# Kernel tuning notes

Hardware: AMD Instinct MI355X
Metric: run time of the kernel (lower is better)

## Reference

```python
import jax, jax.numpy as jnp
import numpy as np

HEADS = 8


def setup_inputs() -> dict:
    key = jax.random.key(0)
    k1, k2, k3 = jax.random.split(key, 3)
    b, n, d = 4, 2048, 256
    x = jax.random.normal(k1, (b, n, d), dtype=jnp.float32)
    # torch Linear weight is [out, in]; we store transposed [in, out] for x @ W
    w_qkv = jax.random.normal(k2, (d, 3 * d), dtype=jnp.float32) * (d ** -0.5)
    b_qkv = jnp.zeros((3 * d,), dtype=jnp.float32)
    w_out = jax.random.normal(k3, (d, d), dtype=jnp.float32) * (d ** -0.5)
    b_out = jnp.zeros((d,), dtype=jnp.float32)
    return {"x": x, "w_qkv": w_qkv, "b_qkv": b_qkv, "w_out": w_out, "b_out": b_out}


def reference(x, w_qkv, b_qkv, w_out, b_out):
    b, n, d = x.shape
    h = HEADS
    dh = d // h
    scale = d ** -0.5  # NOTE: original scales by full dim**-0.5, not head_dim
    qkv = x @ w_qkv + b_qkv                      # [b, n, 3d]
    q, k, v = jnp.split(qkv, 3, axis=-1)         # each [b, n, d]
    to_heads = lambda t: t.reshape(b, n, h, dh).transpose(0, 2, 1, 3)  # [b,h,n,dh]
    q, k, v = to_heads(q), to_heads(k), to_heads(v)
    dots = jnp.einsum('bhid,bhjd->bhij', q, k) * scale   # [b,h,n,n]
    attn = jax.nn.softmax(dots, axis=-1)
    out = jnp.einsum('bhij,bhjd->bhid', attn, v)         # [b,h,n,dh]
    out = out.transpose(0, 2, 1, 3).reshape(b, n, d)     # [b,n,d]
    return out @ w_out + b_out  # dropout is identity in eval mode
```

## Files before the change

kernel.cpp:

```cpp
#include <hip/hip_runtime.h>
#include <hip/hip_bf16.h>
#include <math.h>

#define BATCH  4
#define SEQ    2048
#define DMODEL 256
#define NH     8
#define DH     32
#define MTOT   (BATCH*SEQ)
#define QSCALE 0.09016844005556021f

typedef short  bf16x8 __attribute__((ext_vector_type(8)));
typedef float  f32x4  __attribute__((ext_vector_type(4)));

static __device__ __forceinline__ ushort f2bf(float f) {
    __hip_bfloat16 h = __float2bfloat16(f);
    return __builtin_bit_cast(ushort, h);
}

static __device__ __forceinline__ uint rne2(float a, float b) {
    uint ua = __builtin_bit_cast(uint, a);
    uint ub = __builtin_bit_cast(uint, b);
    ua += 0x7FFFu + ((ua >> 16) & 1u);
    ub += 0x7FFFu + ((ub >> 16) & 1u);
    return __builtin_amdgcn_perm(ub, ua, 0x07060302);
}

__global__ __launch_bounds__(256) void wcvt_all(
    const float* __restrict__ wq, const float* __restrict__ wo,
    const float* __restrict__ x,
    ushort* __restrict__ wqT, ushort* __restrict__ woT,
    ushort* __restrict__ xbf)
{
    const int t  = threadIdx.x;
    const int bx = blockIdx.x;
    if (bx >= 32) {
        const size_t base = ((size_t)(bx - 32) * 8 + blockIdx.y) * 4096 + t * 16;
        float4 f0 = *(const float4*)(x + base);
        float4 f1 = *(const float4*)(x + base + 4);
        float4 f2 = *(const float4*)(x + base + 8);
        float4 f3 = *(const float4*)(x + base + 12);
        uint4 w0, w1;
        w0.x = rne2(f0.x, f0.y); w0.y = rne2(f0.z, f0.w);
        w0.z = rne2(f1.x, f1.y); w0.w = rne2(f1.z, f1.w);
        w1.x = rne2(f2.x, f2.y); w1.y = rne2(f2.z, f2.w);
        w1.z = rne2(f3.x, f3.y); w1.w = rne2(f3.z, f3.w);
        *(uint4*)&xbf[base]     = w0;
        *(uint4*)&xbf[base + 8] = w1;
        return;
    }
    __shared__ float T[32][33];
    const float* w; ushort* wT; int N, n0;
    if (bx < 24) { w = wq; wT = wqT; N = 768; n0 = bx * 32; }
    else         { w = wo; wT = woT; N = 256; n0 = (bx - 24) * 32; }
    const int k0 = blockIdx.y * 32;
    {
        int tr = t >> 3, tc = (t & 7) * 4;
        *(float4*)&T[tr][tc] = *(const float4*)(w + (size_t)(k0 + tr) * N + n0 + tc);
    }
    __syncthreads();
    int nl = t >> 3, kq = (t & 7) * 4;
    ushort4 pk;
    pk.x = f2bf(T[kq + 0][nl]); pk.y = f2bf(T[kq + 1][nl]);
    pk.z = f2bf(T[kq + 2][nl]); pk.w = f2bf(T[kq + 3][nl]);
    *(ushort4*)&wT[(size_t)(n0 + nl) * 256 + k0 + kq] = pk;
}

#define LSQ 72

__global__ __launch_bounds__(256, 3) void qkv_gemm(
    const ushort* __restrict__ xb_, const ushort* __restrict__ wT,
    const float* __restrict__ bias,
    ushort* __restrict__ qo, ushort* __restrict__ ko, ushort* __restrict__ vo)
{
    __shared__ ushort As[64 * LSQ];
    __shared__ ushort Bs[128 * LSQ];
    const int tid  = threadIdx.x;
    const int wid  = tid >> 6;
    const int lane = tid & 63;
    const int lq   = lane & 15;
    const int quad = lane >> 4;
    const int wm   = wid & 1;
    const int wn   = wid >> 1;
    const int m0   = blockIdx.y * 64;
    const int n0   = blockIdx.x * 128;
    const bool isV = (blockIdx.x >= 4);

    const int ar0 = tid >> 3,         ac0 = (tid & 7) * 8;
    const int ar1 = (tid + 256) >> 3, ac1 = ac0;
    const int br0 = tid >> 3,         bc0 = (tid & 7) * 8;
    const int br1 = (tid + 256) >> 3, bc1 = bc0;
    const int br2 = (tid + 512) >> 3, bc2 = bc0;
    const int br3 = (tid + 768) >> 3, bc3 = bc0;

    const ushort* xb = xb_ + (size_t)m0 * 256;
    const ushort* wb = wT  + (size_t)n0 * 256;

    f32x4 acc[8];
#pragma unroll
    for (int i = 0; i < 8; ++i) acc[i] = {0.f, 0.f, 0.f, 0.f};

    uint4 ra0 = *(const uint4*)(xb + (size_t)ar0 * 256 + ac0);
    uint4 ra1 = *(const uint4*)(xb + (size_t)ar1 * 256 + ac1);
    uint4 rb0 = *(const uint4*)(wb + (size_t)br0 * 256 + bc0);
    uint4 rb1 = *(const uint4*)(wb + (size_t)br1 * 256 + bc1);
    uint4 rb2 = *(const uint4*)(wb + (size_t)br2 * 256 + bc2);
    uint4 rb3 = *(const uint4*)(wb + (size_t)br3 * 256 + bc3);

    for (int k0 = 0; k0 < 256; k0 += 64) {
        __syncthreads();
        *(uint4*)&As[ar0 * LSQ + ac0] = ra0;
        *(uint4*)&As[ar1 * LSQ + ac1] = ra1;
        *(uint4*)&Bs[br0 * LSQ + bc0] = rb0;
        *(uint4*)&Bs[br1 * LSQ + bc1] = rb1;
        *(uint4*)&Bs[br2 * LSQ + bc2] = rb2;
        *(uint4*)&Bs[br3 * LSQ + bc3] = rb3;
        __syncthreads();

        const int kn = (k0 + 64) & 255;
        ra0 = *(const uint4*)(xb + (size_t)ar0 * 256 + kn + ac0);
        ra1 = *(const uint4*)(xb + (size_t)ar1 * 256 + kn + ac1);
        rb0 = *(const uint4*)(wb + (size_t)br0 * 256 + kn + bc0);
        rb1 = *(const uint4*)(wb + (size_t)br1 * 256 + kn + bc1);
        rb2 = *(const uint4*)(wb + (size_t)br2 * 256 + kn + bc2);
        rb3 = *(const uint4*)(wb + (size_t)br3 * 256 + kn + bc3);

#pragma unroll
        for (int kh = 0; kh < 2; ++kh) {
            bf16x8 af[2], bfg[4];
#pragma unroll
            for (int mi = 0; mi < 2; ++mi)
                af[mi]  = *(const bf16x8*)&As[(wm * 32 + mi * 16 + lq) * LSQ + kh * 32 + quad * 8];
#pragma unroll
            for (int ni = 0; ni < 4; ++ni)
                bfg[ni] = *(const bf16x8*)&Bs[(wn * 64 + ni * 16 + lq) * LSQ + kh * 32 + quad * 8];
            if (isV) {
#pragma unroll
                for (int mi = 0; mi < 2; ++mi)
#pragma unroll
                    for (int ni = 0; ni < 4; ++ni)
                        acc[mi * 4 + ni] = __builtin_amdgcn_mfma_f32_16x16x32_bf16(
                            af[mi], bfg[ni], acc[mi * 4 + ni], 0, 0, 0);
            } else {
#pragma unroll
                for (int ni = 0; ni < 4; ++ni)
#pragma unroll
                    for (int mi = 0; mi < 2; ++mi)
                        acc[ni * 2 + mi] = __builtin_amdgcn_mfma_f32_16x16x32_bf16(
                            bfg[ni], af[mi], acc[ni * 2 + mi], 0, 0, 0);
            }
        }
    }

    if (!isV) {
#pragma unroll
        for (int ni = 0; ni < 4; ++ni) {
            int nb = n0 + wn * 64 + ni * 16 + quad * 4;
            float4 bs = *(const float4*)(bias + nb);
            int h   = (nb >> 5) & 7;
            int dh0 = nb & 31;
            bool  isQ = (nb < 256);
            float sc  = isQ ? QSCALE : 1.0f;
            ushort* dst = isQ ? qo : ko;
#pragma unroll
            for (int mi = 0; mi < 2; ++mi) {
                int m   = m0 + wm * 32 + mi * 16 + lq;
                int b   = m >> 11, seq = m & 2047;
                f32x4 c = acc[ni * 2 + mi];
                ushort4 pk;
                pk.x = f2bf((c[0] + bs.x) * sc); pk.y = f2bf((c[1] + bs.y) * sc);
                pk.z = f2bf((c[2] + bs.z) * sc); pk.w = f2bf((c[3] + bs.w) * sc);
                *(ushort4*)&dst[(((size_t)b * NH + h) * SEQ + seq) * DH + dh0] = pk;
            }
        }
    } else {
#pragma unroll
        for (int ni = 0; ni < 4; ++ni) {
            int n  = n0 + wn * 64 + ni * 16 + lq;
            int h  = (n >> 5) & 7;
            int dh = n & 31;
            float bsc = bias[n];
#pragma unroll
            for (int mi = 0; mi < 2; ++mi) {
                int mb  = m0 + wm * 32 + mi * 16 + quad * 4;
                int b   = mb >> 11, seq = mb & 2047;
                f32x4 c = acc[mi * 4 + ni];
                ushort4 pk;
                pk.x = f2bf(c[0] + bsc); pk.y = f2bf(c[1] + bsc);
                pk.z = f2bf(c[2] + bsc); pk.w = f2bf(c[3] + bsc);
                *(ushort4*)&vo[(((size_t)b * NH + h) * DH + dh) * SEQ + seq] = pk;
            }
        }
    }
}

#define KS_STRIDE 40
#define VT_STRIDE 136
#define P_STRIDE  136

__global__ __launch_bounds__(256, 4) void attn_mfma(
    const ushort* __restrict__ qb, const ushort* __restrict__ kb,
    const ushort* __restrict__ vtb, ushort* __restrict__ a_bf)
{
    __shared__ ushort Ks[128 * KS_STRIDE];
    __shared__ ushort VsT[32 * VT_STRIDE];
    __shared__ ushort Pl[4 * 32 * P_STRIDE];

    const int tid  = threadIdx.x;
    const int wid  = tid >> 6;
    const int lane = tid & 63;
    const int lq   = lane & 15;
    const int quad = lane >> 4;
    const int h    = blockIdx.y;
    const int b    = blockIdx.z;
    const int bh   = b * NH + h;
    const int q0   = blockIdx.x * 128 + wid * 32;

    const ushort* qbase = qb + ((size_t)bh * SEQ + q0) * DH;
    const bf16x8 qf0 = *(const bf16x8*)(qbase + (size_t)lq * DH + quad * 8);
    const bf16x8 qf1 = *(const bf16x8*)(qbase + (size_t)(16 + lq) * DH + quad * 8);

    const ushort* kbase  = kb  + (size_t)bh * SEQ * DH;
    const ushort* vtbase = vtb + (size_t)bh * DH * SEQ;
    ushort* Pw = Pl + wid * 32 * P_STRIDE;

    const int f0 = tid, f1 = tid + 256;
    const int kgo0 = (f0 >> 2) * DH + (f0 & 3) * 8;
    const int kgo1 = (f1 >> 2) * DH + (f1 & 3) * 8;
    const int klo0 = (f0 >> 2) * KS_STRIDE + (f0 & 3) * 8;
    const int klo1 = (f1 >> 2) * KS_STRIDE + (f1 & 3) * 8;
    const int vgo0 = (f0 >> 4) * SEQ + (f0 & 15) * 8;
    const int vgo1 = (f1 >> 4) * SEQ + (f1 & 15) * 8;
    const int vlo0 = (f0 >> 4) * VT_STRIDE + (f0 & 15) * 8;
    const int vlo1 = (f1 >> 4) * VT_STRIDE + (f1 & 15) * 8;

    uint4 kr0 = *(const uint4*)(kbase  + kgo0);
    uint4 kr1 = *(const uint4*)(kbase  + kgo1);
    uint4 vr0 = *(const uint4*)(vtbase + vgo0);
    uint4 vr1 = *(const uint4*)(vtbase + vgo1);

    f32x4 o0 = {0.f, 0.f, 0.f, 0.f};
    f32x4 o1 = {0.f, 0.f, 0.f, 0.f};
    f32x4 o2 = {0.f, 0.f, 0.f, 0.f};
    f32x4 o3 = {0.f, 0.f, 0.f, 0.f};
    float l0 = 0.f, l1 = 0.f;

    for (int kt = 0; kt < SEQ; kt += 128) {
        __syncthreads();
        *(uint4*)&Ks[klo0]  = kr0;
        *(uint4*)&Ks[klo1]  = kr1;
        *(uint4*)&VsT[vlo0] = vr0;
        *(uint4*)&VsT[vlo1] = vr1;
        __syncthreads();

        {
            const int ktn = (kt + 128) & (SEQ - 1);
            const ushort* kn = kbase  + (size_t)ktn * DH;
            const ushort* vn = vtbase + ktn;
            kr0 = *(const uint4*)(kn + kgo0);
            kr1 = *(const uint4*)(kn + kgo1);
            vr0 = *(const uint4*)(vn + vgo0);
            vr1 = *(const uint4*)(vn + vgo1);
        }

        {
            f32x4 st[8];
#pragma unroll
            for (int t = 0; t < 8; ++t) {
                bf16x8 kf = *(const bf16x8*)&Ks[(t * 16 + lq) * KS_STRIDE + quad * 8];
                f32x4 z = {0.f, 0.f, 0.f, 0.f};
                st[t] = __builtin_amdgcn_mfma_f32_16x16x32_bf16(kf, qf0, z, 0, 0, 0);
            }
#pragma unroll
            for (int t = 0; t < 8; ++t) {
                float p0 = __builtin_amdgcn_exp2f(st[t][0]);
                float p1 = __builtin_amdgcn_exp2f(st[t][1]);
                float p2 = __builtin_amdgcn_exp2f(st[t][2]);
                float p3 = __builtin_amdgcn_exp2f(st[t][3]);
                l0 += (p0 + p1) + (p2 + p3);
                uint2 w;
                w.x = rne2(p0, p1);
                w.y = rne2(p2, p3);
                *(uint2*)&Pw[lq * P_STRIDE + t * 16 + quad * 4] = w;
            }
        }
        {
            f32x4 st[8];
#pragma unroll
            for (int t = 0; t < 8; ++t) {
                bf16x8 kf = *(const bf16x8*)&Ks[(t * 16 + lq) * KS_STRIDE + quad * 8];
                f32x4 z = {0.f, 0.f, 0.f, 0.f};
                st[t] = __builtin_amdgcn_mfma_f32_16x16x32_bf16(kf, qf1, z, 0, 0, 0);
            }
#pragma unroll
            for (int t = 0; t < 8; ++t) {
                float p0 = __builtin_amdgcn_exp2f(st[t][0]);
                float p1 = __builtin_amdgcn_exp2f(st[t][1]);
                float p2 = __builtin_amdgcn_exp2f(st[t][2]);
                float p3 = __builtin_amdgcn_exp2f(st[t][3]);
                l1 += (p0 + p1) + (p2 + p3);
                uint2 w;
                w.x = rne2(p0, p1);
                w.y = rne2(p2, p3);
                *(uint2*)&Pw[(16 + lq) * P_STRIDE + t * 16 + quad * 4] = w;
            }
        }

#pragma unroll
        for (int s = 0; s < 4; ++s) {
            bf16x8 v0 = *(const bf16x8*)&VsT[lq        * VT_STRIDE + s * 32 + quad * 8];
            bf16x8 v1 = *(const bf16x8*)&VsT[(16 + lq) * VT_STRIDE + s * 32 + quad * 8];
            bf16x8 p0 = *(const bf16x8*)&Pw[lq        * P_STRIDE + s * 32 + quad * 8];
            bf16x8 p1 = *(const bf16x8*)&Pw[(16 + lq) * P_STRIDE + s * 32 + quad * 8];
            o0 = __builtin_amdgcn_mfma_f32_16x16x32_bf16(v0, p0, o0, 0, 0, 0);
            o1 = __builtin_amdgcn_mfma_f32_16x16x32_bf16(v1, p0, o1, 0, 0, 0);
            o2 = __builtin_amdgcn_mfma_f32_16x16x32_bf16(v0, p1, o2, 0, 0, 0);
            o3 = __builtin_amdgcn_mfma_f32_16x16x32_bf16(v1, p1, o3, 0, 0, 0);
        }
    }

    l0 += __shfl_xor(l0, 16); l0 += __shfl_xor(l0, 32);
    l1 += __shfl_xor(l1, 16); l1 += __shfl_xor(l1, 32);
    float inv0 = 1.0f / l0;
    float inv1 = 1.0f / l1;
    ushort* dst0 = a_bf + ((size_t)b * SEQ + q0 + lq) * DMODEL + h * DH;
    ushort* dst1 = dst0 + 16 * DMODEL;
    uint2 w0, w1;
    w0.x = rne2(o0[0] * inv0, o0[1] * inv0);
    w0.y = rne2(o0[2] * inv0, o0[3] * inv0);
    w1.x = rne2(o1[0] * inv0, o1[1] * inv0);
    w1.y = rne2(o1[2] * inv0, o1[3] * inv0);
    *(uint2*)&dst0[quad * 4]      = w0;
    *(uint2*)&dst0[16 + quad * 4] = w1;
    w0.x = rne2(o2[0] * inv1, o2[1] * inv1);
    w0.y = rne2(o2[2] * inv1, o2[3] * inv1);
    w1.x = rne2(o3[0] * inv1, o3[1] * inv1);
    w1.y = rne2(o3[2] * inv1, o3[3] * inv1);
    *(uint2*)&dst1[quad * 4]      = w0;
    *(uint2*)&dst1[16 + quad * 4] = w1;
}

__global__ __launch_bounds__(256) void out_gemm(
    const ushort* __restrict__ a, const ushort* __restrict__ wT,
    const float* __restrict__ bias, float* __restrict__ out)
{
    __shared__ ushort As[64 * LSQ];
    __shared__ ushort Bs[64 * LSQ];
    const int tid  = threadIdx.x;
    const int wid  = tid >> 6;
    const int lane = tid & 63;
    const int lq   = lane & 15;
    const int quad = lane >> 4;
    const int wm   = wid & 1;
    const int wn   = wid >> 1;
    const int m0   = blockIdx.y * 64;
    const int n0   = blockIdx.x * 64;

    const int f0 = tid, f1 = tid + 256;
    const int r0 = f0 >> 3, c0 = (f0 & 7) * 8;
    const int r1 = f1 >> 3, c1 = (f1 & 7) * 8;

    const ushort* ab = a  + (size_t)m0 * 256;
    const ushort* wb = wT + (size_t)n0 * 256;

    f32x4 acc[4];
#pragma unroll
    for (int i = 0; i < 4; ++i) acc[i] = {0.f, 0.f, 0.f, 0.f};

    uint4 ra0 = *(const uint4*)(ab + (size_t)r0 * 256 + c0);
    uint4 ra1 = *(const uint4*)(ab + (size_t)r1 * 256 + c1);
    uint4 rb0 = *(const uint4*)(wb + (size_t)r0 * 256 + c0);
    uint4 rb1 = *(const uint4*)(wb + (size_t)r1 * 256 + c1);

    for (int k0 = 0; k0 < 256; k0 += 64) {
        __syncthreads();
        *(uint4*)&As[r0 * LSQ + c0] = ra0;
        *(uint4*)&As[r1 * LSQ + c1] = ra1;
        *(uint4*)&Bs[r0 * LSQ + c0] = rb0;
        *(uint4*)&Bs[r1 * LSQ + c1] = rb1;
        __syncthreads();

        const int kn = (k0 + 64) & 255;
        ra0 = *(const uint4*)(ab + (size_t)r0 * 256 + kn + c0);
        ra1 = *(const uint4*)(ab + (size_t)r1 * 256 + kn + c1);
        rb0 = *(const uint4*)(wb + (size_t)r0 * 256 + kn + c0);
        rb1 = *(const uint4*)(wb + (size_t)r1 * 256 + kn + c1);

#pragma unroll
        for (int kh = 0; kh < 2; ++kh) {
            bf16x8 af[2], bfg[2];
#pragma unroll
            for (int mi = 0; mi < 2; ++mi)
                af[mi]  = *(const bf16x8*)&As[(wm * 32 + mi * 16 + lq) * LSQ + kh * 32 + quad * 8];
#pragma unroll
            for (int ni = 0; ni < 2; ++ni)
                bfg[ni] = *(const bf16x8*)&Bs[(wn * 32 + ni * 16 + lq) * LSQ + kh * 32 + quad * 8];
#pragma unroll
            for (int ni = 0; ni < 2; ++ni)
#pragma unroll
                for (int mi = 0; mi < 2; ++mi)
                    acc[ni * 2 + mi] = __builtin_amdgcn_mfma_f32_16x16x32_bf16(
                        bfg[ni], af[mi], acc[ni * 2 + mi], 0, 0, 0);
        }
    }

#pragma unroll
    for (int ni = 0; ni < 2; ++ni) {
        int nb = n0 + wn * 32 + ni * 16 + quad * 4;
        float4 bs = *(const float4*)(bias + nb);
#pragma unroll
        for (int mi = 0; mi < 2; ++mi) {
            int m = m0 + wm * 32 + mi * 16 + lq;
            f32x4 c = acc[ni * 2 + mi];
            float4 o;
            o.x = c[0] + bs.x; o.y = c[1] + bs.y;
            o.z = c[2] + bs.z; o.w = c[3] + bs.w;
            *(float4*)&out[(size_t)m * DMODEL + nb] = o;
        }
    }
}

extern "C" void kernel_launch(void* const* d_in, const int* in_sizes, int n_in,
                              void* d_out, int out_size, void* d_ws, size_t ws_size,
                              hipStream_t stream) {
    const float* x     = (const float*)d_in[0];
    const float* w_qkv = (const float*)d_in[1];
    const float* b_qkv = (const float*)d_in[2];
    const float* w_out = (const float*)d_in[3];
    const float* b_out = (const float*)d_in[4];
    float* out = (float*)d_out;

    const size_t TSZ = (size_t)MTOT * DMODEL;
    ushort* q_ws = (ushort*)d_ws;
    ushort* k_ws = q_ws + TSZ;
    ushort* v_ws = k_ws + TSZ;
    ushort* a_bf = v_ws + TSZ;
    ushort* xbf  = a_bf + TSZ;
    ushort* wqT  = xbf + TSZ;
    ushort* woT  = wqT + 768 * 256;

    wcvt_all<<<dim3(96, 8), 256, 0, stream>>>(w_qkv, w_out, x, wqT, woT, xbf);
    qkv_gemm<<<dim3(6, 128), 256, 0, stream>>>(xbf, wqT, b_qkv, q_ws, k_ws, v_ws);
    attn_mfma<<<dim3(SEQ / 128, NH, BATCH), 256, 0, stream>>>(
        q_ws, k_ws, v_ws, a_bf);
    out_gemm<<<dim3(4, 128), 256, 0, stream>>>(a_bf, woT, b_out, out);
}
```

Measured before the change: 124.2 us.

## Fuse all MHA stages into one cooperative persistent kernel with grid syncs

Replaces the four separate launches (weight/x conversion, QKV GEMM, attention, output GEMM) with a single cooperative kernel of 512 blocks. The stages are separated by grid.sync() calls, and the x-to-bf16 conversion is folded into the QKV GEMM's A-tile load. The goal is to remove launch gaps, the tail effects between kernels, and the separate x conversion pass. In exchange, each stage is limited to 512 blocks with launch_bounds(256,2), which may lower attention occupancy. The four-kernel path is kept as a fallback if the cooperative launch fails.

```diff
diff --git a/kernel.cpp b/kernel.cpp
--- a/kernel.cpp
+++ b/kernel.cpp
@@ -1,6 +1,9 @@
 #include <hip/hip_runtime.h>
 #include <hip/hip_bf16.h>
+#include <hip/hip_cooperative_groups.h>
 #include <math.h>
+
+namespace cg = cooperative_groups;
 
 #define BATCH  4
 #define SEQ    2048
@@ -17,13 +20,390 @@
     __hip_bfloat16 h = __float2bfloat16(f);
     return __builtin_bit_cast(ushort, h);
 }
-
 static __device__ __forceinline__ uint rne2(float a, float b) {
     uint ua = __builtin_bit_cast(uint, a);
     uint ub = __builtin_bit_cast(uint, b);
     ua += 0x7FFFu + ((ua >> 16) & 1u);
     ub += 0x7FFFu + ((ub >> 16) & 1u);
     return __builtin_amdgcn_perm(ub, ua, 0x07060302);
+}
+
+#define LSQ 72
+#define KS_STRIDE 40
+#define VT_STRIDE 136
+#define P_STRIDE  136
+
+__global__ void __launch_bounds__(256, 2) fused_mha(
+    const float* __restrict__ x,  const float* __restrict__ wq,
+    const float* __restrict__ wo, const float* __restrict__ bq,
+    const float* __restrict__ bo, float* __restrict__ out,
+    ushort* __restrict__ wqT, ushort* __restrict__ woT,
+    ushort* __restrict__ q_ws, ushort* __restrict__ k_ws,
+    ushort* __restrict__ v_ws, ushort* __restrict__ a_bf)
+{
+    __shared__ __align__(16) ushort smem[26880];
+    cg::grid_group grid = cg::this_grid();
+    const int bid  = blockIdx.x;
+    const int tid  = threadIdx.x;
+    const int wid  = tid >> 6;
+    const int lane = tid & 63;
+    const int lq   = lane & 15;
+    const int quad = lane >> 4;
+
+    if (bid < 256) {
+        float* T = (float*)smem;
+        const float* w; ushort* wT; int N, n0, k0;
+        if (bid < 192) { w = wq; wT = wqT; N = 768; n0 = (bid % 24) * 32; k0 = (bid / 24) * 32; }
+        else { int i2 = bid - 192; w = wo; wT = woT; N = 256; n0 = (i2 % 8) * 32; k0 = (i2 / 8) * 32; }
+        {
+            int tr = tid >> 3, tc = (tid & 7) * 4;
+            *(float4*)&T[tr * 33 + tc] = *(const float4*)(w + (size_t)(k0 + tr) * N + n0 + tc);
+        }
+        __syncthreads();
+        int nl = tid >> 3, kq = (tid & 7) * 4;
+        ushort4 pk;
+        pk.x = f2bf(T[(kq + 0) * 33 + nl]); pk.y = f2bf(T[(kq + 1) * 33 + nl]);
+        pk.z = f2bf(T[(kq + 2) * 33 + nl]); pk.w = f2bf(T[(kq + 3) * 33 + nl]);
+        *(ushort4*)&wT[(size_t)(n0 + nl) * 256 + k0 + kq] = pk;
+    }
+    grid.sync();
+
+    {
+        ushort* As = smem;
+        ushort* Bs = smem + 64 * LSQ;
+        const int wm = wid & 1;
+        const int wn = wid >> 1;
+        const int ar0 = tid >> 4,         ac0 = (tid & 15) * 4;
+        const int ar1 = (tid + 256) >> 4;
+        const int ar2 = (tid + 512) >> 4;
+        const int ar3 = (tid + 768) >> 4;
+        const int br0 = tid >> 3,         bc0 = (tid & 7) * 8;
+        const int br1 = (tid + 256) >> 3;
+        const int br2 = (tid + 512) >> 3;
+        const int br3 = (tid + 768) >> 3;
+
+        for (int it = bid; it < 768; it += 512) {
+            const int m0  = (it / 6) * 64;
+            const int n0  = (it % 6) * 128;
+            const bool isV = ((it % 6) >= 4);
+            const float*  xb = x   + (size_t)m0 * 256;
+            const ushort* wb = wqT + (size_t)n0 * 256;
+
+            f32x4 acc[8];
+#pragma unroll
+            for (int i = 0; i < 8; ++i) acc[i] = {0.f, 0.f, 0.f, 0.f};
+
+            float4 ra0 = *(const float4*)(xb + (size_t)ar0 * 256 + ac0);
+            float4 ra1 = *(const float4*)(xb + (size_t)ar1 * 256 + ac0);
+            float4 ra2 = *(const float4*)(xb + (size_t)ar2 * 256 + ac0);
+            float4 ra3 = *(const float4*)(xb + (size_t)ar3 * 256 + ac0);
+            uint4  rb0 = *(const uint4*)(wb + (size_t)br0 * 256 + bc0);
+            uint4  rb1 = *(const uint4*)(wb + (size_t)br1 * 256 + bc0);
+            uint4  rb2 = *(const uint4*)(wb + (size_t)br2 * 256 + bc0);
+            uint4  rb3 = *(const uint4*)(wb + (size_t)br3 * 256 + bc0);
+
+            for (int k0 = 0; k0 < 256; k0 += 64) {
+                __syncthreads();
+                {
+                    uint2 w2;
+                    w2.x = rne2(ra0.x, ra0.y); w2.y = rne2(ra0.z, ra0.w);
+                    *(uint2*)&As[ar0 * LSQ + ac0] = w2;
+                    w2.x = rne2(ra1.x, ra1.y); w2.y = rne2(ra1.z, ra1.w);
+                    *(uint2*)&As[ar1 * LSQ + ac0] = w2;
+                    w2.x = rne2(ra2.x, ra2.y); w2.y = rne2(ra2.z, ra2.w);
+                    *(uint2*)&As[ar2 * LSQ + ac0] = w2;
+                    w2.x = rne2(ra3.x, ra3.y); w2.y = rne2(ra3.z, ra3.w);
+                    *(uint2*)&As[ar3 * LSQ + ac0] = w2;
+                }
+                *(uint4*)&Bs[br0 * LSQ + bc0] = rb0;
+                *(uint4*)&Bs[br1 * LSQ + bc0] = rb1;
+                *(uint4*)&Bs[br2 * LSQ + bc0] = rb2;
+                *(uint4*)&Bs[br3 * LSQ + bc0] = rb3;
+                __syncthreads();
+
+                const int kn = (k0 + 64) & 255;
+                ra0 = *(const float4*)(xb + (size_t)ar0 * 256 + kn + ac0);
+                ra1 = *(const float4*)(xb + (size_t)ar1 * 256 + kn + ac0);
+                ra2 = *(const float4*)(xb + (size_t)ar2 * 256 + kn + ac0);
+                ra3 = *(const float4*)(xb + (size_t)ar3 * 256 + kn + ac0);
+                rb0 = *(const uint4*)(wb + (size_t)br0 * 256 + kn + bc0);
+                rb1 = *(const uint4*)(wb + (size_t)br1 * 256 + kn + bc0);
+                rb2 = *(const uint4*)(wb + (size_t)br2 * 256 + kn + bc0);
+                rb3 = *(const uint4*)(wb + (size_t)br3 * 256 + kn + bc0);
+
+#pragma unroll
+                for (int kh = 0; kh < 2; ++kh) {
+                    bf16x8 af[2], bfg[4];
+#pragma unroll
+                    for (int mi = 0; mi < 2; ++mi)
+                        af[mi]  = *(const bf16x8*)&As[(wm * 32 + mi * 16 + lq) * LSQ + kh * 32 + quad * 8];
+#pragma unroll
+                    for (int ni = 0; ni < 4; ++ni)
+                        bfg[ni] = *(const bf16x8*)&Bs[(wn * 64 + ni * 16 + lq) * LSQ + kh * 32 + quad * 8];
+                    if (isV) {
+#pragma unroll
+                        for (int mi = 0; mi < 2; ++mi)
+#pragma unroll
+                            for (int ni = 0; ni < 4; ++ni)
+                                acc[mi * 4 + ni] = __builtin_amdgcn_mfma_f32_16x16x32_bf16(
+                                    af[mi], bfg[ni], acc[mi * 4 + ni], 0, 0, 0);
+                    } else {
+#pragma unroll
+                        for (int ni = 0; ni < 4; ++ni)
+#pragma unroll
+                            for (int mi = 0; mi < 2; ++mi)
+                                acc[ni * 2 + mi] = __builtin_amdgcn_mfma_f32_16x16x32_bf16(
+                                    bfg[ni], af[mi], acc[ni * 2 + mi], 0, 0, 0);
+                    }
+                }
+            }
+
+            if (!isV) {
+#pragma unroll
+                for (int ni = 0; ni < 4; ++ni) {
+                    int nb = n0 + wn * 64 + ni * 16 + quad * 4;
+                    float4 bs = *(const float4*)(bq + nb);
+                    int h   = (nb >> 5) & 7;
+                    int dh0 = nb & 31;
+                    bool  isQ = (nb < 256);
+                    float sc  = isQ ? QSCALE : 1.0f;
+                    ushort* dst = isQ ? q_ws : k_ws;
+#pragma unroll
+                    for (int mi = 0; mi < 2; ++mi) {
+                        int m   = m0 + wm * 32 + mi * 16 + lq;
+                        int b   = m >> 11, seq = m & 2047;
+                        f32x4 c = acc[ni * 2 + mi];
+                        ushort4 pk;
+                        pk.x = f2bf((c[0] + bs.x) * sc); pk.y = f2bf((c[1] + bs.y) * sc);
+                        pk.z = f2bf((c[2] + bs.z) * sc); pk.w = f2bf((c[3] + bs.w) * sc);
+                        *(ushort4*)&dst[(((size_t)b * NH + h) * SEQ + seq) * DH + dh0] = pk;
+                    }
+                }
+            } else {
+#pragma unroll
+                for (int ni = 0; ni < 4; ++ni) {
+                    int n  = n0 + wn * 64 + ni * 16 + lq;
+                    int h  = (n >> 5) & 7;
+                    int dh = n & 31;
+                    float bsc = bq[n];
+#pragma unroll
+                    for (int mi = 0; mi < 2; ++mi) {
+                        int mb  = m0 + wm * 32 + mi * 16 + quad * 4;
+                        int b   = mb >> 11, seq = mb & 2047;
+                        f32x4 c = acc[mi * 4 + ni];
+                        ushort4 pk;
+                        pk.x = f2bf(c[0] + bsc); pk.y = f2bf(c[1] + bsc);
+                        pk.z = f2bf(c[2] + bsc); pk.w = f2bf(c[3] + bsc);
+                        *(ushort4*)&v_ws[(((size_t)b * NH + h) * DH + dh) * SEQ + seq] = pk;
+                    }
+                }
+            }
+            __syncthreads();
+        }
+    }
+    grid.sync();
+
+    {
+        ushort* Ks  = smem;
+        ushort* VsT = smem + 128 * KS_STRIDE;
+        ushort* Pl  = VsT + 32 * VT_STRIDE;
+
+        const int qt = bid & 15;
+        const int h  = (bid >> 4) & 7;
+        const int b  = bid >> 7;
+        const int bh = b * NH + h;
+        const int q0 = qt * 128 + wid * 32;
+
+        const ushort* qbase = q_ws + ((size_t)bh * SEQ + q0) * DH;
+        const bf16x8 qf0 = *(const bf16x8*)(qbase + (size_t)lq * DH + quad * 8);
+        const bf16x8 qf1 = *(const bf16x8*)(qbase + (size_t)(16 + lq) * DH + quad * 8);
+
+        const ushort* kbase  = k_ws + (size_t)bh * SEQ * DH;
+        const ushort* vtbase = v_ws + (size_t)bh * DH * SEQ;
+        ushort* Pw = Pl + wid * 32 * P_STRIDE;
+
+        const int f0 = tid, f1 = tid + 256;
+        const int kgo0 = (f0 >> 2) * DH + (f0 & 3) * 8;
+        const int kgo1 = (f1 >> 2) * DH + (f1 & 3) * 8;
+        const int klo0 = (f0 >> 2) * KS_STRIDE + (f0 & 3) * 8;
+        const int klo1 = (f1 >> 2) * KS_STRIDE + (f1 & 3) * 8;
+        const int vgo0 = (f0 >> 4) * SEQ + (f0 & 15) * 8;
+        const int vgo1 = (f1 >> 4) * SEQ + (f1 & 15) * 8;
+        const int vlo0 = (f0 >> 4) * VT_STRIDE + (f0 & 15) * 8;
+        const int vlo1 = (f1 >> 4) * VT_STRIDE + (f1 & 15) * 8;
+
+        uint4 kr0 = *(const uint4*)(kbase  + kgo0);
+        uint4 kr1 = *(const uint4*)(kbase  + kgo1);
+        uint4 vr0 = *(const uint4*)(vtbase + vgo0);
+        uint4 vr1 = *(const uint4*)(vtbase + vgo1);
+
+        f32x4 o0 = {0.f,0.f,0.f,0.f}, o1 = {0.f,0.f,0.f,0.f};
+        f32x4 o2 = {0.f,0.f,0.f,0.f}, o3 = {0.f,0.f,0.f,0.f};
+        float l0 = 0.f, l1 = 0.f;
+
+        for (int kt = 0; kt < SEQ; kt += 128) {
+            __syncthreads();
+            *(uint4*)&Ks[klo0]  = kr0;
+            *(uint4*)&Ks[klo1]  = kr1;
+            *(uint4*)&VsT[vlo0] = vr0;
+            *(uint4*)&VsT[vlo1] = vr1;
+            __syncthreads();
+
+            {
+                const int ktn = (kt + 128) & (SEQ - 1);
+                const ushort* kn = kbase  + (size_t)ktn * DH;
+                const ushort* vn = vtbase + ktn;
+                kr0 = *(const uint4*)(kn + kgo0);
+                kr1 = *(const uint4*)(kn + kgo1);
+                vr0 = *(const uint4*)(vn + vgo0);
+                vr1 = *(const uint4*)(vn + vgo1);
+            }
+
+            {
+                f32x4 st[8];
+#pragma unroll
+                for (int t = 0; t < 8; ++t) {
+                    bf16x8 kf = *(const bf16x8*)&Ks[(t * 16 + lq) * KS_STRIDE + quad * 8];
+                    f32x4 z = {0.f, 0.f, 0.f, 0.f};
+                    st[t] = __builtin_amdgcn_mfma_f32_16x16x32_bf16(kf, qf0, z, 0, 0, 0);
+                }
+#pragma unroll
+                for (int t = 0; t < 8; ++t) {
+                    float p0 = __builtin_amdgcn_exp2f(st[t][0]);
+                    float p1 = __builtin_amdgcn_exp2f(st[t][1]);
+                    float p2 = __builtin_amdgcn_exp2f(st[t][2]);
+                    float p3 = __builtin_amdgcn_exp2f(st[t][3]);
+                    l0 += (p0 + p1) + (p2 + p3);
+                    uint2 w2; w2.x = rne2(p0, p1); w2.y = rne2(p2, p3);
+                    *(uint2*)&Pw[lq * P_STRIDE + t * 16 + quad * 4] = w2;
+                }
+            }
+            {
+                f32x4 st[8];
+#pragma unroll
+                for (int t = 0; t < 8; ++t) {
+                    bf16x8 kf = *(const bf16x8*)&Ks[(t * 16 + lq) * KS_STRIDE + quad * 8];
+                    f32x4 z = {0.f, 0.f, 0.f, 0.f};
+                    st[t] = __builtin_amdgcn_mfma_f32_16x16x32_bf16(kf, qf1, z, 0, 0, 0);
+                }
+#pragma unroll
+                for (int t = 0; t < 8; ++t) {
+                    float p0 = __builtin_amdgcn_exp2f(st[t][0]);
+                    float p1 = __builtin_amdgcn_exp2f(st[t][1]);
+                    float p2 = __builtin_amdgcn_exp2f(st[t][2]);
+                    float p3 = __builtin_amdgcn_exp2f(st[t][3]);
+                    l1 += (p0 + p1) + (p2 + p3);
+                    uint2 w2; w2.x = rne2(p0, p1); w2.y = rne2(p2, p3);
+                    *(uint2*)&Pw[(16 + lq) * P_STRIDE + t * 16 + quad * 4] = w2;
+                }
+            }
+
+#pragma unroll
+            for (int s = 0; s < 4; ++s) {
+                bf16x8 v0 = *(const bf16x8*)&VsT[lq        * VT_STRIDE + s * 32 + quad * 8];
+                bf16x8 v1 = *(const bf16x8*)&VsT[(16 + lq) * VT_STRIDE + s * 32 + quad * 8];
+                bf16x8 p0 = *(const bf16x8*)&Pw[lq        * P_STRIDE + s * 32 + quad * 8];
+                bf16x8 p1 = *(const bf16x8*)&Pw[(16 + lq) * P_STRIDE + s * 32 + quad * 8];
+                o0 = __builtin_amdgcn_mfma_f32_16x16x32_bf16(v0, p0, o0, 0, 0, 0);
+                o1 = __builtin_amdgcn_mfma_f32_16x16x32_bf16(v1, p0, o1, 0, 0, 0);
+                o2 = __builtin_amdgcn_mfma_f32_16x16x32_bf16(v0, p1, o2, 0, 0, 0);
+                o3 = __builtin_amdgcn_mfma_f32_16x16x32_bf16(v1, p1, o3, 0, 0, 0);
+            }
+        }
+
+        l0 += __shfl_xor(l0, 16); l0 += __shfl_xor(l0, 32);
+        l1 += __shfl_xor(l1, 16); l1 += __shfl_xor(l1, 32);
+        float inv0 = 1.0f / l0;
+        float inv1 = 1.0f / l1;
+        ushort* dst0 = a_bf + ((size_t)b * SEQ + q0 + lq) * DMODEL + h * DH;
+        ushort* dst1 = dst0 + 16 * DMODEL;
+        uint2 w0, w1;
+        w0.x = rne2(o0[0] * inv0, o0[1] * inv0);
+        w0.y = rne2(o0[2] * inv0, o0[3] * inv0);
+        w1.x = rne2(o1[0] * inv0, o1[1] * inv0);
+        w1.y = rne2(o1[2] * inv0, o1[3] * inv0);
+        *(uint2*)&dst0[quad * 4]      = w0;
+        *(uint2*)&dst0[16 + quad * 4] = w1;
+        w0.x = rne2(o2[0] * inv1, o2[1] * inv1);
+        w0.y = rne2(o2[2] * inv1, o2[3] * inv1);
+        w1.x = rne2(o3[0] * inv1, o3[1] * inv1);
+        w1.y = rne2(o3[2] * inv1, o3[3] * inv1);
+        *(uint2*)&dst1[quad * 4]      = w0;
+        *(uint2*)&dst1[16 + quad * 4] = w1;
+    }
+    grid.sync();
+
+    {
+        ushort* As = smem;
+        ushort* Bs = smem + 64 * LSQ;
+        const int wm = wid & 1;
+        const int wn = wid >> 1;
+        const int m0 = (bid >> 2) * 64;
+        const int n0 = (bid & 3) * 64;
+
+        const int f0 = tid, f1 = tid + 256;
+        const int r0 = f0 >> 3, c0 = (f0 & 7) * 8;
+        const int r1 = f1 >> 3, c1 = (f1 & 7) * 8;
+
+        const ushort* ab = a_bf + (size_t)m0 * 256;
+        const ushort* wb = woT  + (size_t)n0 * 256;
+
+        f32x4 acc[4];
+#pragma unroll
+        for (int i = 0; i < 4; ++i) acc[i] = {0.f, 0.f, 0.f, 0.f};
+
+        uint4 ra0 = *(const uint4*)(ab + (size_t)r0 * 256 + c0);
+        uint4 ra1 = *(const uint4*)(ab + (size_t)r1 * 256 + c1);
+        uint4 rb0 = *(const uint4*)(wb + (size_t)r0 * 256 + c0);
+        uint4 rb1 = *(const uint4*)(wb + (size_t)r1 * 256 + c1);
+
+        for (int k0 = 0; k0 < 256; k0 += 64) {
+            __syncthreads();
+            *(uint4*)&As[r0 * LSQ + c0] = ra0;
+            *(uint4*)&As[r1 * LSQ + c1] = ra1;
+            *(uint4*)&Bs[r0 * LSQ + c0] = rb0;
+            *(uint4*)&Bs[r1 * LSQ + c1] = rb1;
+            __syncthreads();
+
+            const int kn = (k0 + 64) & 255;
+            ra0 = *(const uint4*)(ab + (size_t)r0 * 256 + kn + c0);
+            ra1 = *(const uint4*)(ab + (size_t)r1 * 256 + kn + c1);
+            rb0 = *(const uint4*)(wb + (size_t)r0 * 256 + kn + c0);
+            rb1 = *(const uint4*)(wb + (size_t)r1 * 256 + kn + c1);
+
+#pragma unroll
+            for (int kh = 0; kh < 2; ++kh) {
+                bf16x8 af[2], bfg[2];
+#pragma unroll
+                for (int mi = 0; mi < 2; ++mi)
+                    af[mi]  = *(const bf16x8*)&As[(wm * 32 + mi * 16 + lq) * LSQ + kh * 32 + quad * 8];
+#pragma unroll
+                for (int ni = 0; ni < 2; ++ni)
+                    bfg[ni] = *(const bf16x8*)&Bs[(wn * 32 + ni * 16 + lq) * LSQ + kh * 32 + quad * 8];
+#pragma unroll
+                for (int ni = 0; ni < 2; ++ni)
+#pragma unroll
+                    for (int mi = 0; mi < 2; ++mi)
+                        acc[ni * 2 + mi] = __builtin_amdgcn_mfma_f32_16x16x32_bf16(
+                            bfg[ni], af[mi], acc[ni * 2 + mi], 0, 0, 0);
+            }
+        }
+
+#pragma unroll
+        for (int ni = 0; ni < 2; ++ni) {
+            int nb = n0 + wn * 32 + ni * 16 + quad * 4;
+            float4 bs = *(const float4*)(bo + nb);
+#pragma unroll
+            for (int mi = 0; mi < 2; ++mi) {
+                int m = m0 + wm * 32 + mi * 16 + lq;
+                f32x4 c = acc[ni * 2 + mi];
+                float4 o;
+                o.x = c[0] + bs.x; o.y = c[1] + bs.y;
+                o.z = c[2] + bs.z; o.w = c[3] + bs.w;
+                *(float4*)&out[(size_t)m * DMODEL + nb] = o;
+            }
+        }
+    }
 }
 
 __global__ __launch_bounds__(256) void wcvt_all(
@@ -66,8 +446,6 @@
     *(ushort4*)&wT[(size_t)(n0 + nl) * 256 + k0 + kq] = pk;
 }
 
-#define LSQ 72
-
 __global__ __launch_bounds__(256, 3) void qkv_gemm(
     const ushort* __restrict__ xb_, const ushort* __restrict__ wT,
     const float* __restrict__ bias,
@@ -87,11 +465,11 @@
     const bool isV = (blockIdx.x >= 4);
 
     const int ar0 = tid >> 3,         ac0 = (tid & 7) * 8;
-    const int ar1 = (tid + 256) >> 3, ac1 = ac0;
+    const int ar1 = (tid + 256) >> 3;
     const int br0 = tid >> 3,         bc0 = (tid & 7) * 8;
-    const int br1 = (tid + 256) >> 3, bc1 = bc0;
-    const int br2 = (tid + 512) >> 3, bc2 = bc0;
-    const int br3 = (tid + 768) >> 3, bc3 = bc0;
+    const int br1 = (tid + 256) >> 3;
+    const int br2 = (tid + 512) >> 3;
+    const int br3 = (tid + 768) >> 3;
 
     const ushort* xb = xb_ + (size_t)m0 * 256;
     const ushort* wb = wT  + (size_t)n0 * 256;
@@ -101,29 +479,29 @@
     for (int i = 0; i < 8; ++i) acc[i] = {0.f, 0.f, 0.f, 0.f};
 
     uint4 ra0 = *(const uint4*)(xb + (size_t)ar0 * 256 + ac0);
-    uint4 ra1 = *(const uint4*)(xb + (size_t)ar1 * 256 + ac1);
+    uint4 ra1 = *(const uint4*)(xb + (size_t)ar1 * 256 + ac0);
     uint4 rb0 = *(const uint4*)(wb + (size_t)br0 * 256 + bc0);
-    uint4 rb1 = *(const uint4*)(wb + (size_t)br1 * 256 + bc1);
-    uint4 rb2 = *(const uint4*)(wb + (size_t)br2 * 256 + bc2);
-    uint4 rb3 = *(const uint4*)(wb + (size_t)br3 * 256 + bc3);
+    uint4 rb1 = *(const uint4*)(wb + (size_t)br1 * 256 + bc0);
+    uint4 rb2 = *(const uint4*)(wb + (size_t)br2 * 256 + bc0);
+    uint4 rb3 = *(const uint4*)(wb + (size_t)br3 * 256 + bc0);
 
     for (int k0 = 0; k0 < 256; k0 += 64) {
         __syncthreads();
         *(uint4*)&As[ar0 * LSQ + ac0] = ra0;
-        *(uint4*)&As[ar1 * LSQ + ac1] = ra1;
+        *(uint4*)&As[ar1 * LSQ + ac0] = ra1;
         *(uint4*)&Bs[br0 * LSQ + bc0] = rb0;
-        *(uint4*)&Bs[br1 * LSQ + bc1] = rb1;
-        *(uint4*)&Bs[br2 * LSQ + bc2] = rb2;
-        *(uint4*)&Bs[br3 * LSQ + bc3] = rb3;
+        *(uint4*)&Bs[br1 * LSQ + bc0] = rb1;
+        *(uint4*)&Bs[br2 * LSQ + bc0] = rb2;
+        *(uint4*)&Bs[br3 * LSQ + bc0] = rb3;
         __syncthreads();
 
         const int kn = (k0 + 64) & 255;
         ra0 = *(const uint4*)(xb + (size_t)ar0 * 256 + kn + ac0);
-        ra1 = *(const uint4*)(xb + (size_t)ar1 * 256 + kn + ac1);
+        ra1 = *(const uint4*)(xb + (size_t)ar1 * 256 + kn + ac0);
         rb0 = *(const uint4*)(wb + (size_t)br0 * 256 + kn + bc0);
-        rb1 = *(const uint4*)(wb + (size_t)br1 * 256 + kn + bc1);
-        rb2 = *(const uint4*)(wb + (size_t)br2 * 256 + kn + bc2);
-        rb3 = *(const uint4*)(wb + (size_t)br3 * 256 + kn + bc3);
+        rb1 = *(const uint4*)(wb + (size_t)br1 * 256 + kn + bc0);
+        rb2 = *(const uint4*)(wb + (size_t)br2 * 256 + kn + bc0);
+        rb3 = *(const uint4*)(wb + (size_t)br3 * 256 + kn + bc0);
 
 #pragma unroll
         for (int kh = 0; kh < 2; ++kh) {
@@ -193,10 +571,6 @@
         }
     }
 }
-
-#define KS_STRIDE 40
-#define VT_STRIDE 136
-#define P_STRIDE  136
 
 __global__ __launch_bounds__(256, 4) void attn_mfma(
     const ushort* __restrict__ qb, const ushort* __restrict__ kb,
@@ -239,10 +613,8 @@
     uint4 vr0 = *(const uint4*)(vtbase + vgo0);
     uint4 vr1 = *(const uint4*)(vtbase + vgo1);
 
-    f32x4 o0 = {0.f, 0.f, 0.f, 0.f};
-    f32x4 o1 = {0.f, 0.f, 0.f, 0.f};
-    f32x4 o2 = {0.f, 0.f, 0.f, 0.f};
-    f32x4 o3 = {0.f, 0.f, 0.f, 0.f};
+    f32x4 o0 = {0.f,0.f,0.f,0.f}, o1 = {0.f,0.f,0.f,0.f};
+    f32x4 o2 = {0.f,0.f,0.f,0.f}, o3 = {0.f,0.f,0.f,0.f};
     float l0 = 0.f, l1 = 0.f;
 
     for (int kt = 0; kt < SEQ; kt += 128) {
@@ -278,10 +650,8 @@
                 float p2 = __builtin_amdgcn_exp2f(st[t][2]);
                 float p3 = __builtin_amdgcn_exp2f(st[t][3]);
                 l0 += (p0 + p1) + (p2 + p3);
-                uint2 w;
-                w.x = rne2(p0, p1);
-                w.y = rne2(p2, p3);
-                *(uint2*)&Pw[lq * P_STRIDE + t * 16 + quad * 4] = w;
+                uint2 w2; w2.x = rne2(p0, p1); w2.y = rne2(p2, p3);
+                *(uint2*)&Pw[lq * P_STRIDE + t * 16 + quad * 4] = w2;
             }
         }
         {
@@ -299,10 +669,8 @@
                 float p2 = __builtin_amdgcn_exp2f(st[t][2]);
                 float p3 = __builtin_amdgcn_exp2f(st[t][3]);
                 l1 += (p0 + p1) + (p2 + p3);
-                uint2 w;
-                w.x = rne2(p0, p1);
-                w.y = rne2(p2, p3);
-                *(uint2*)&Pw[(16 + lq) * P_STRIDE + t * 16 + quad * 4] = w;
+                uint2 w2; w2.x = rne2(p0, p1); w2.y = rne2(p2, p3);
+                *(uint2*)&Pw[(16 + lq) * P_STRIDE + t * 16 + quad * 4] = w2;
             }
         }
 
@@ -439,9 +807,18 @@
     ushort* wqT  = xbf + TSZ;
     ushort* woT  = wqT + 768 * 256;
 
-    wcvt_all<<<dim3(96, 8), 256, 0, stream>>>(w_qkv, w_out, x, wqT, woT, xbf);
-    qkv_gemm<<<dim3(6, 128), 256, 0, stream>>>(xbf, wqT, b_qkv, q_ws, k_ws, v_ws);
-    attn_mfma<<<dim3(SEQ / 128, NH, BATCH), 256, 0, stream>>>(
-        q_ws, k_ws, v_ws, a_bf);
-    out_gemm<<<dim3(4, 128), 256, 0, stream>>>(a_bf, woT, b_out, out);
+    void* args[] = {
+        (void*)&x, (void*)&w_qkv, (void*)&w_out, (void*)&b_qkv, (void*)&b_out,
+        (void*)&out, (void*)&wqT, (void*)&woT,
+        (void*)&q_ws, (void*)&k_ws, (void*)&v_ws, (void*)&a_bf
+    };
+    hipError_t err = hipLaunchCooperativeKernel((void*)fused_mha, dim3(512),
+                                                dim3(256), args, 0, stream);
+    if (err != hipSuccess) {
+        wcvt_all<<<dim3(96, 8), 256, 0, stream>>>(w_qkv, w_out, x, wqT, woT, xbf);
+        qkv_gemm<<<dim3(6, 128), 256, 0, stream>>>(xbf, wqT, b_qkv, q_ws, k_ws, v_ws);
+        attn_mfma<<<dim3(SEQ / 128, NH, BATCH), 256, 0, stream>>>(
+            q_ws, k_ws, v_ws, a_bf);
+        out_gemm<<<dim3(4, 128), 256, 0, stream>>>(a_bf, woT, b_out, out);
+    }
 }
```

Result: slower. 311.3 us (+150.6%).
